# Kernel optimization log

Measured on AMD Instinct MI355X. Metric: run time of the kernel, lower is better.

The kernel has to match this reference:

```python
import jax, jax.numpy as jnp
import numpy as np

WINDOW_SIZE = 11
SIGMA = 1.5
C1 = 0.01 ** 2
C2 = 0.03 ** 2


def _gaussian_window(window_size, sigma, channel):
    x = np.arange(window_size)
    g = np.exp(-((x - window_size // 2) ** 2) / (2.0 * sigma ** 2))
    g = g / g.sum()
    w2d = np.outer(g, g).astype(np.float32)  # [K,K]
    # depthwise kernel [C,1,K,K] (OIHW with feature_group_count=C)
    return jnp.asarray(np.broadcast_to(w2d, (channel, 1, window_size, window_size)))


def _depthwise_conv(x, window):
    # x: [B,C,H,W], window: [C,1,K,K]; SAME padding, groups=C
    pad = WINDOW_SIZE // 2
    return jax.lax.conv_general_dilated(
        x, window,
        window_strides=(1, 1),
        padding=[(pad, pad), (pad, pad)],
        dimension_numbers=('NCHW', 'OIHW', 'NCHW'),
        feature_group_count=x.shape[1],
    )


def setup_inputs() -> dict:
    key = jax.random.key(0)
    k1, k2 = jax.random.split(key)
    shape = (16, 3, 512, 512)
    img1 = jax.random.uniform(k1, shape, dtype=jnp.float32)
    img2 = jax.random.uniform(k2, shape, dtype=jnp.float32)
    return {"img1": img1, "img2": img2}


def reference(img1, img2):
    channel = img1.shape[1]
    window = _gaussian_window(WINDOW_SIZE, SIGMA, channel).astype(img1.dtype)

    mu1 = _depthwise_conv(img1, window)
    mu2 = _depthwise_conv(img2, window)
    mu1_sq = mu1 * mu1
    mu2_sq = mu2 * mu2
    mu1_mu2 = mu1 * mu2

    sigma1_sq = _depthwise_conv(img1 * img1, window) - mu1_sq
    sigma2_sq = _depthwise_conv(img2 * img2, window) - mu2_sq
    sigma12 = _depthwise_conv(img1 * img2, window) - mu1_mu2

    ssim_map = ((2 * mu1_mu2 + C1) * (2 * sigma12 + C2)) / (
        (mu1_sq + mu2_sq + C1) * (sigma1_sq + sigma2_sq + C2))
    # size_average=True -> scalar mean
    return jnp.mean(ssim_map)
```

## Files before the change

kernel.cpp:

```cpp
#include <hip/hip_runtime.h>

#define IMG 512
#define NPLANES 48
#define TW 64
#define TH 32
#define RD 5
#define KW 11
#define VC (TW + 2*RD)
#define PRW (2*VC)
#define NTX (IMG/TW)
#define NTY (IMG/TH)
#define TPP (NTX*NTY)
#define NBLOCKS (NPLANES*TPP)
#define NPIX (16.0f*3.0f*512.0f*512.0f)

typedef float v2f __attribute__((ext_vector_type(2)));

__device__ __forceinline__ v2f pk_fma(v2f a, v2f b, v2f c) {
    v2f d;
    asm("v_pk_fma_f32 %0, %1, %2, %3" : "=v"(d) : "v"(a), "v"(b), "v"(c));
    return d;
}
__device__ __forceinline__ v2f pk_mul(v2f a, v2f b) {
    v2f d;
    asm("v_pk_mul_f32 %0, %1, %2" : "=v"(d) : "v"(a), "v"(b));
    return d;
}
__device__ __forceinline__ v2f pk_sd(float a, float b) {
    v2f d;
    d.x = a + b;
    d.y = a - b;
    return d;
}

__device__ __forceinline__ float fast_rcp(float d) {
    float r = __builtin_amdgcn_rcpf(d);
    r = r * (2.0f - d * r);
    return r;
}

__global__ __launch_bounds__(256) void ssim_kernel(
    const float* __restrict__ img1, const float* __restrict__ img2,
    float* __restrict__ partial)
{
    __shared__ __align__(16) float vSD[TH][PRW];
    __shared__ __align__(16) float vQ [TH][PRW];
    __shared__ float wsum[4];

    const v2f cw2[KW] = {
        {0.00102838f,0.00102838f}, {0.00759876f,0.00759876f},
        {0.03600077f,0.03600077f}, {0.10936069f,0.10936069f},
        {0.21300553f,0.21300553f}, {0.26601172f,0.26601172f},
        {0.21300553f,0.21300553f}, {0.10936069f,0.10936069f},
        {0.03600077f,0.03600077f}, {0.00759876f,0.00759876f},
        {0.00102838f,0.00102838f}
    };

    const int tid = threadIdx.x;
    const int blk = blockIdx.x;
    const int plane = blk / TPP;
    const int t     = blk % TPP;
    const int ty0 = (t / NTX) * TH;
    const int tx0 = (t % NTX) * TW;
    const float* __restrict__ p1 = img1 + (size_t)plane * IMG * IMG;
    const float* __restrict__ p2 = img2 + (size_t)plane * IMG * IMG;

    const bool interior = (tx0 >= RD) && (tx0 + TW + RD <= IMG) &&
                          (ty0 >= RD) && (ty0 + TH + RD <= IMG);

    if (tid < VC * 2) {
        const int col = tid % VC;
        const int sp  = tid / VC;
        const int gx  = tx0 + col - RD;
        const int r0  = sp * 16;

        float a[26], b[26];
        if (interior) {
            const unsigned off0 = (unsigned)((ty0 + r0 - RD) * IMG + gx);
            #pragma unroll
            for (int k = 0; k < 26; k++) {
                a[k] = p1[off0 + (unsigned)(k * IMG)];
                b[k] = p2[off0 + (unsigned)(k * IMG)];
            }
        } else {
            const bool xok = (gx >= 0) && (gx < IMG);
            #pragma unroll
            for (int k = 0; k < 26; k++) {
                const int gy = ty0 + r0 + k - RD;
                const bool ok = xok && (gy >= 0) && (gy < IMG);
                const int gi = gy * IMG + gx;
                a[k] = ok ? p1[gi] : 0.f;
                b[k] = ok ? p2[gi] : 0.f;
            }
        }

        v2f sSD[16], sQ[16];
        #pragma unroll
        for (int k = 0; k < 26; k++) {
            const v2f sd = pk_sd(a[k], b[k]);
            const v2f q  = pk_mul(sd, sd);
            #pragma unroll
            for (int o = 0; o < 16; o++) {
                const int d = k - o;
                if (d == 0) {
                    sSD[o] = pk_mul(cw2[0], sd);
                    sQ[o]  = pk_mul(cw2[0], q);
                } else if (d > 0 && d < KW) {
                    sSD[o] = pk_fma(cw2[d], sd, sSD[o]);
                    sQ[o]  = pk_fma(cw2[d], q,  sQ[o]);
                }
            }
        }

        #pragma unroll
        for (int o = 0; o < 16; o++) {
            const int r = r0 + o;
            *(v2f*)&vSD[r][2 * col] = sSD[o];
            *(v2f*)&vQ [r][2 * col] = sQ[o];
        }
    }
    __syncthreads();

    const float C1 = 1e-4f;
    const float C2 = 9e-4f;
    const v2f NEG1 = {-1.f, -1.f};
    float acc = 0.f;
    {
        const int j = tid & 7;
        const int r = tid >> 3;

        v2f prSD[18], prQ[18];
        {
            const float4* rowp = (const float4*)&vSD[r][0];
            #pragma unroll
            for (int i = 0; i < 9; i++) {
                const float4 q = rowp[4 * j + i];
                prSD[2 * i]     = (v2f){q.x, q.y};
                prSD[2 * i + 1] = (v2f){q.z, q.w};
            }
        }
        {
            const float4* rowp = (const float4*)&vQ[r][0];
            #pragma unroll
            for (int i = 0; i < 9; i++) {
                const float4 q = rowp[4 * j + i];
                prQ[2 * i]     = (v2f){q.x, q.y};
                prQ[2 * i + 1] = (v2f){q.z, q.w};
            }
        }

        #pragma unroll
        for (int o = 0; o < 8; o++) {
            v2f M = pk_mul(cw2[0], prSD[o]);
            v2f X = pk_mul(cw2[0], prQ[o]);
            #pragma unroll
            for (int d = 1; d < KW; d++) {
                M = pk_fma(cw2[d], prSD[o + d], M);
                X = pk_fma(cw2[d], prQ[o + d], X);
            }
            const v2f M2 = pk_mul(M, M);
            const v2f V  = pk_fma(M2, NEG1, X);
            const float mm = M2.x - M2.y;
            const float mp = M2.x + M2.y;
            const float vm = V.x - V.y;
            const float vp = V.x + V.y;
            const float num = fmaf(0.5f, mm, C1) * fmaf(0.5f, vm, C2);
            const float den = fmaf(0.5f, mp, C1) * fmaf(0.5f, vp, C2);
            acc += num * fast_rcp(den);
        }
    }

    #pragma unroll
    for (int off = 32; off > 0; off >>= 1)
        acc += __shfl_down(acc, off, 64);
    const int lane = tid & 63;
    const int wv_i = tid >> 6;
    if (lane == 0) wsum[wv_i] = acc;
    __syncthreads();
    if (tid == 0)
        partial[blk] = (wsum[0] + wsum[1]) + (wsum[2] + wsum[3]);
}

__global__ __launch_bounds__(256) void ssim_reduce_kernel(
    const float* __restrict__ partial, float* __restrict__ out)
{
    float acc = 0.f;
    for (int i = threadIdx.x; i < NBLOCKS; i += 256)
        acc += partial[i];
    #pragma unroll
    for (int off = 32; off > 0; off >>= 1)
        acc += __shfl_down(acc, off, 64);
    __shared__ float wsum[4];
    const int lane = threadIdx.x & 63;
    const int wv_i = threadIdx.x >> 6;
    if (lane == 0) wsum[wv_i] = acc;
    __syncthreads();
    if (threadIdx.x == 0)
        out[0] = ((wsum[0] + wsum[1]) + (wsum[2] + wsum[3])) * (1.0f / NPIX);
}

extern "C" void kernel_launch(void* const* d_in, const int* in_sizes, int n_in,
                              void* d_out, int out_size, void* d_ws, size_t ws_size,
                              hipStream_t stream) {
    const float* img1 = (const float*)d_in[0];
    const float* img2 = (const float*)d_in[1];
    float* out = (float*)d_out;
    float* partial = (float*)d_ws;

    ssim_kernel<<<NBLOCKS, 256, 0, stream>>>(img1, img2, partial);
    ssim_reduce_kernel<<<1, 256, 0, stream>>>(partial, out);
}
```

Before: 146.4 us.

## Process two vertical tiles per block, prefetching the second tile during pass two

Each block now covers two stacked 64x32 tiles, which halves the grid and the per-block overhead. The global loads for the second tile are issued before the horizontal pass on the first tile, so that memory latency overlaps with compute. This costs extra registers for the second set of 52 prefetched floats, which may lower occupancy, and adds two more barriers per block.

```diff
diff --git a/kernel.cpp b/kernel.cpp
--- a/kernel.cpp
+++ b/kernel.cpp
@@ -4,13 +4,14 @@
 #define NPLANES 48
 #define TW 64
 #define TH 32
+#define TPAIR 64
 #define RD 5
 #define KW 11
 #define VC (TW + 2*RD)
 #define PRW (2*VC)
 #define NTX (IMG/TW)
-#define NTY (IMG/TH)
-#define TPP (NTX*NTY)
+#define NTYP (IMG/TPAIR)
+#define TPP (NTX*NTYP)
 #define NBLOCKS (NPLANES*TPP)
 #define NPIX (16.0f*3.0f*512.0f*512.0f)
 
@@ -60,23 +61,22 @@
     const int blk = blockIdx.x;
     const int plane = blk / TPP;
     const int t     = blk % TPP;
-    const int ty0 = (t / NTX) * TH;
+    const int ty0 = (t / NTX) * TPAIR;
     const int tx0 = (t % NTX) * TW;
     const float* __restrict__ p1 = img1 + (size_t)plane * IMG * IMG;
     const float* __restrict__ p2 = img2 + (size_t)plane * IMG * IMG;
 
-    const bool interior = (tx0 >= RD) && (tx0 + TW + RD <= IMG) &&
-                          (ty0 >= RD) && (ty0 + TH + RD <= IMG);
-
-    if (tid < VC * 2) {
-        const int col = tid % VC;
-        const int sp  = tid / VC;
-        const int gx  = tx0 + col - RD;
-        const int r0  = sp * 16;
-
-        float a[26], b[26];
-        if (interior) {
-            const unsigned off0 = (unsigned)((ty0 + r0 - RD) * IMG + gx);
+    const bool xint   = (tx0 >= RD) && (tx0 + TW + RD <= IMG);
+    const bool p1task = (tid < VC * 2);
+    const int col = tid % VC;
+    const int sp  = tid / VC;
+    const int gx  = tx0 + col - RD;
+
+    auto load_tile = [&](int ty, float* a, float* b) {
+        if (!p1task) return;
+        const int r0 = sp * 16;
+        if (xint && (ty >= RD) && (ty + TH + RD <= IMG)) {
+            const unsigned off0 = (unsigned)((ty + r0 - RD) * IMG + gx);
             #pragma unroll
             for (int k = 0; k < 26; k++) {
                 a[k] = p1[off0 + (unsigned)(k * IMG)];
@@ -86,14 +86,18 @@
             const bool xok = (gx >= 0) && (gx < IMG);
             #pragma unroll
             for (int k = 0; k < 26; k++) {
-                const int gy = ty0 + r0 + k - RD;
+                const int gy = ty + r0 + k - RD;
                 const bool ok = xok && (gy >= 0) && (gy < IMG);
                 const int gi = gy * IMG + gx;
                 a[k] = ok ? p1[gi] : 0.f;
                 b[k] = ok ? p2[gi] : 0.f;
             }
         }
-
+    };
+
+    auto conv_store = [&](const float* a, const float* b) {
+        if (!p1task) return;
+        const int r0 = sp * 16;
         v2f sSD[16], sQ[16];
         #pragma unroll
         for (int k = 0; k < 26; k++) {
@@ -111,24 +115,20 @@
                 }
             }
         }
-
         #pragma unroll
         for (int o = 0; o < 16; o++) {
             const int r = r0 + o;
             *(v2f*)&vSD[r][2 * col] = sSD[o];
             *(v2f*)&vQ [r][2 * col] = sQ[o];
         }
-    }
-    __syncthreads();
+    };
 
     const float C1 = 1e-4f;
     const float C2 = 9e-4f;
     const v2f NEG1 = {-1.f, -1.f};
-    float acc = 0.f;
-    {
+    auto pass2 = [&](float& accr) {
         const int j = tid & 7;
         const int r = tid >> 3;
-
         v2f prSD[18], prQ[18];
         {
             const float4* rowp = (const float4*)&vSD[r][0];
@@ -148,7 +148,6 @@
                 prQ[2 * i + 1] = (v2f){q.z, q.w};
             }
         }
-
         #pragma unroll
         for (int o = 0; o < 8; o++) {
             v2f M = pk_mul(cw2[0], prSD[o]);
@@ -166,9 +165,22 @@
             const float vp = V.x + V.y;
             const float num = fmaf(0.5f, mm, C1) * fmaf(0.5f, vm, C2);
             const float den = fmaf(0.5f, mp, C1) * fmaf(0.5f, vp, C2);
-            acc += num * fast_rcp(den);
-        }
-    }
+            accr += num * fast_rcp(den);
+        }
+    };
+
+    float a0[26], b0[26], a1[26], b1[26];
+    float acc = 0.f;
+
+    load_tile(ty0, a0, b0);
+    conv_store(a0, b0);
+    __syncthreads();
+    load_tile(ty0 + TH, a1, b1);
+    pass2(acc);
+    __syncthreads();
+    conv_store(a1, b1);
+    __syncthreads();
+    pass2(acc);
 
     #pragma unroll
     for (int off = 32; off > 0; off >>= 1)
```

Result: no change. 144.8 us (-1.1%).
